# Performance work log

Measured on AMD Instinct MI355X. Metric: run time of the kernel, lower is better.

Reference implementation:

```python
import jax, jax.numpy as jnp
import numpy as np

CIN, HID, OUT = 128, 256, 349
NTYPES, ETYPES = 4, 5
N0, N1, N2 = 120000, 40000, 10000
GNODES, GEDGES = 250000, 2000000
E0, E1 = 1500000, 400000


def setup_inputs() -> dict:
    key = jax.random.key(0)
    ks = jax.random.split(key, 24)
    ri = jax.random.randint
    rn = jax.random.normal
    inp = {}
    inp['n_id'] = ri(ks[0], (N0,), 0, GNODES)
    inp['x0'] = rn(ks[1], (100000, CIN), dtype=jnp.float32)
    inp['src0'] = ri(ks[2], (E0,), 0, N0)
    inp['dst0'] = ri(ks[3], (E0,), 0, N1)
    inp['e_id0'] = ri(ks[4], (E0,), 0, GEDGES)
    inp['src1'] = ri(ks[5], (E1,), 0, N1)
    inp['dst1'] = ri(ks[6], (E1,), 0, N2)
    inp['e_id1'] = ri(ks[7], (E1,), 0, GEDGES)
    inp['edge_type'] = ri(ks[8], (GEDGES,), 0, ETYPES)
    inp['node_type'] = ri(ks[9], (GNODES,), 0, NTYPES)
    inp['local_node_idx'] = ri(ks[10], (GNODES,), 0, 50000)
    # learned parameters
    inp['emb1'] = rn(ks[11], (50000, CIN), dtype=jnp.float32)
    inp['emb2'] = rn(ks[12], (50000, CIN), dtype=jnp.float32)
    inp['emb3'] = rn(ks[13], (50000, CIN), dtype=jnp.float32)
    s0 = 1.0 / np.sqrt(CIN)
    s1 = 1.0 / np.sqrt(HID)
    inp['relW0'] = rn(ks[14], (ETYPES, CIN, HID), dtype=jnp.float32) * s0
    inp['rootW0'] = rn(ks[15], (NTYPES, CIN, HID), dtype=jnp.float32) * s0
    inp['rootb0'] = rn(ks[16], (NTYPES, HID), dtype=jnp.float32) * 0.02
    inp['relW1'] = rn(ks[17], (ETYPES, HID, OUT), dtype=jnp.float32) * s1
    inp['rootW1'] = rn(ks[18], (NTYPES, HID, OUT), dtype=jnp.float32) * s1
    inp['rootb1'] = rn(ks[19], (NTYPES, OUT), dtype=jnp.float32) * 0.02
    return inp


def _group_input(tables, node_type, local_node_idx, n_id):
    # RGNN.group_input: per-node-type gather from feature / embedding tables.
    nt = node_type[n_id]            # [N0]
    li = local_node_idx[n_id]       # [N0]
    h = jnp.zeros((n_id.shape[0], CIN), dtype=tables[0].dtype)
    for k, tab in enumerate(tables):
        idx = jnp.minimum(li, tab.shape[0] - 1)
        h = jnp.where((nt == k)[:, None], tab[idx], h)
    return h, nt


def _rgcn_layer(x, nt_src, src, dst, et, relW, rootW, rootb, n_tgt):
    # out = sum_t mean-aggregate(x_j over edges of type t) @ W_t  (linear commutes with mean)
    T = relW.shape[0]
    xj = x[src]                                           # [E, Cin] gather
    seg = dst * T + et                                    # fused (target, edge_type) segment id
    sums = jax.ops.segment_sum(xj, seg, num_segments=n_tgt * T)
    cnts = jax.ops.segment_sum(jnp.ones((src.shape[0],), x.dtype), seg, num_segments=n_tgt * T)
    mean = (sums / jnp.maximum(cnts, 1.0)[:, None]).reshape(n_tgt, T, -1)  # [Nt, T, Cin]
    out = jnp.einsum('ntc,tco->no', mean, relW)           # [Nt, Cout]
    # per-node-type root linear: out[mask] += root_lins[i](x_target[mask])
    x_t = x[:n_tgt]
    nt_t = nt_src[:n_tgt]
    allr = jnp.einsum('nc,tco->tno', x_t, rootW) + rootb[:, None, :]  # [Tn, Nt, Cout]
    root = jnp.take_along_axis(allr, nt_t[None, :, None], axis=0)[0]
    return out + root


def reference(n_id, x0, src0, dst0, e_id0, src1, dst1, e_id1, edge_type, node_type,
              local_node_idx, emb1, emb2, emb3, relW0, rootW0, rootb0, relW1, rootW1, rootb1):
    h, nt = _group_input([x0, emb1, emb2, emb3], node_type, local_node_idx, n_id)
    # layer 0: I -> H
    h = _rgcn_layer(h, nt, src0, dst0, edge_type[e_id0], relW0, rootW0, rootb0, N1)
    h = jax.nn.relu(h)
    nt = nt[:N1]
    # layer 1: H -> O
    h = _rgcn_layer(h, nt, src1, dst1, edge_type[e_id1], relW1, rootW1, rootb1, N2)
    return jax.nn.log_softmax(h, axis=-1)
```

## Files before the change

### kernel.cpp

```cpp
#include <hip/hip_runtime.h>
#include <hip/hip_bf16.h>
#include <cmath>

constexpr int kCIN = 128, kHID = 256, kOUT = 349;
constexpr int kNT = 4, kET = 5;
constexpr int kN0 = 120000, kN1 = 40000, kN2 = 10000;
constexpr int kNSEG0 = kN1 * kET;
constexpr int kNSEG1 = kN2 * kET;
constexpr int kNSEG = kNSEG0 + kNSEG1;

constexpr int kBinSegs = 512;
constexpr int kNBin0 = (kNSEG0 + kBinSegs - 1) / kBinSegs;
constexpr int kNBin1 = (kNSEG1 + kBinSegs - 1) / kBinSegs;
constexpr int kNBin  = kNBin0 + kNBin1;
constexpr int kNBLK  = 512;
constexpr int kSB    = 128;

typedef __bf16 bf16x8 __attribute__((ext_vector_type(8)));
typedef float f32x4 __attribute__((ext_vector_type(4)));
typedef float f32x2v __attribute__((ext_vector_type(2)));
typedef unsigned short ushort8v __attribute__((ext_vector_type(8)));

__device__ __forceinline__ unsigned short f2b(float f) {
    unsigned int b = __float_as_uint(f);
    unsigned int r = (b + 0x7FFFu + ((b >> 16) & 1u)) >> 16;
    return (unsigned short)r;
}
__device__ __forceinline__ float b2f(unsigned short u) {
    return __uint_as_float((unsigned int)u << 16);
}
__device__ __forceinline__ void gl2lds16(const void* g, void* l) {
    __builtin_amdgcn_global_load_lds(
        (const __attribute__((address_space(1))) void*)g,
        (__attribute__((address_space(3))) void*)l, 16, 0, 0);
}

__device__ __forceinline__ unsigned int f2e4m3(float f) {
#if __has_builtin(__builtin_amdgcn_cvt_pk_fp8_f32)
    return (unsigned int)(__builtin_amdgcn_cvt_pk_fp8_f32(f, f, 0, false) & 0xFF);
#else
    unsigned int sb = (__float_as_uint(f) >> 31) << 7;
    float m = fminf(fabsf(f), 448.f);
    unsigned int code;
    if (m < 0.015625f) {
        code = (unsigned int)__float2int_rn(m * 512.f);
    } else {
        unsigned int b = __float_as_uint(m);
        b = b + 0x7FFFF + ((b >> 20) & 1);
        int e8 = (int)(b >> 23) - 120;
        if (e8 > 15) code = 0x7E;
        else code = ((unsigned int)e8 << 3) | ((b >> 20) & 7);
    }
    return sb | code;
#endif
}

__device__ __forceinline__ void e4m3x4_to_f32(unsigned int u, float* o4) {
#if __has_builtin(__builtin_amdgcn_cvt_pk_f32_fp8)
    f32x2v a = __builtin_amdgcn_cvt_pk_f32_fp8(u, false);
    f32x2v b = __builtin_amdgcn_cvt_pk_f32_fp8(u, true);
    o4[0] = a[0]; o4[1] = a[1]; o4[2] = b[0]; o4[3] = b[1];
#else
#pragma unroll
    for (int i = 0; i < 4; i++) {
        unsigned int c = (u >> (8 * i)) & 0xFF;
        unsigned int s = c >> 7, e = (c >> 3) & 15, mm = c & 7;
        float v;
        if (e == 0) v = (float)mm * 0.001953125f;
        else        v = __uint_as_float((e + 120u) << 23 | mm << 20);
        o4[i] = s ? -v : v;
    }
#endif
}

__global__ void k_prep(const float* __restrict__ relW0, const float* __restrict__ rootW0,
                       unsigned short* __restrict__ Bt0T,
                       const float* __restrict__ relW1, const float* __restrict__ rootW1,
                       unsigned short* __restrict__ Bt1T,
                       const int* __restrict__ etype, unsigned char* __restrict__ et8, int nET)
{
    constexpr int T0 = kNT * 256 * 768;
    constexpr int T1 = kNT * 384 * 1536;
    constexpr int TP = T0 + T1;
    int i = blockIdx.x * 256 + threadIdx.x;
    if (i < T0) {
        int g = i / (256 * 768);
        int rem = i - g * (256 * 768);
        int col = rem / 768;
        int k = rem - col * 768;
        float v = (k < 640) ? relW0[(size_t)k * 256 + col]
                            : rootW0[((size_t)g * 128 + (k - 640)) * 256 + col];
        Bt0T[i] = f2b(v);
    } else if (i < TP) {
        int ii = i - T0;
        int g = ii / (384 * 1536);
        int rem = ii - g * (384 * 1536);
        int col = rem / 1536;
        int k = rem - col * 1536;
        float v = 0.f;
        if (col < kOUT) v = (k < 1280) ? relW1[(size_t)k * kOUT + col]
                                       : rootW1[((size_t)g * 256 + (k - 1280)) * kOUT + col];
        Bt1T[ii] = f2b(v);
    } else {
        int k = i - TP;
        if (k < nET) et8[k] = (unsigned char)etype[k];
    }
}

__global__ void k_gather(const int* __restrict__ n_id, const float* __restrict__ x0,
                         const float* __restrict__ e1, const float* __restrict__ e2,
                         const float* __restrict__ e3, const int* __restrict__ ntype,
                         const int* __restrict__ lidx, unsigned short* __restrict__ h0b,
                         unsigned char* __restrict__ h0f8, int* __restrict__ nt0)
{
    int row = blockIdx.x * 8 + (threadIdx.x >> 5);
    if (row >= kN0) return;
    int lane = threadIdx.x & 31;
    int gid = n_id[row];
    int nt = ntype[gid];
    int li = lidx[gid];
    const float* tab;
    int rows;
    if (nt == 0)      { tab = x0; rows = 100000; }
    else if (nt == 1) { tab = e1; rows = 50000; }
    else if (nt == 2) { tab = e2; rows = 50000; }
    else              { tab = e3; rows = 50000; }
    int idx = li < rows ? li : rows - 1;
    float4 v = reinterpret_cast<const float4*>(tab + (size_t)idx * kCIN)[lane];
    ushort4 o;
    o.x = f2b(v.x); o.y = f2b(v.y); o.z = f2b(v.z); o.w = f2b(v.w);
    reinterpret_cast<ushort4*>(h0b + (size_t)row * kCIN)[lane] = o;
    unsigned int q = f2e4m3(v.x) | (f2e4m3(v.y) << 8) | (f2e4m3(v.z) << 16) | (f2e4m3(v.w) << 24);
    reinterpret_cast<unsigned int*>(h0f8 + (size_t)row * kCIN)[lane] = q;
    if (lane == 0) nt0[row] = nt;
}

__global__ __launch_bounds__(1024) void k_bincnt(
    const int* __restrict__ dst0, const int* __restrict__ eid0, int E0,
    const int* __restrict__ dst1, const int* __restrict__ eid1, int E1,
    const unsigned char* __restrict__ et8, int* __restrict__ cnts2d,
    int* __restrict__ seg32,
    const int* __restrict__ nt0, int* __restrict__ ntcnts)
{
    __shared__ int h[kNBin];
    const int tid = threadIdx.x;
    if (blockIdx.x < kNBLK) {
        for (int k = tid; k < kNBin; k += 1024) h[k] = 0;
        __syncthreads();
        int Etot = E0 + E1;
        int chunk = (Etot + kNBLK - 1) / kNBLK;
        int lo = blockIdx.x * chunk;
        int hi = min(lo + chunk, Etot);
        for (int i = lo + tid; i < hi; i += 1024) {
            int c;
            if (i < E0) c = dst0[i] * kET + (int)et8[eid0[i]];
            else { int e = i - E0; c = kNBin0 * kBinSegs + dst1[e] * kET + (int)et8[eid1[e]]; }
            seg32[i] = c;
            atomicAdd(&h[c >> 9], 1);
        }
        __syncthreads();
        for (int k = tid; k < kNBin; k += 1024) cnts2d[(size_t)k * kNBLK + blockIdx.x] = h[k];
    } else {
        int b = blockIdx.x - kNBLK;
        int layer = b >= kSB;
        int blk = b - layer * kSB;
        int M = layer ? kN2 : kN1;
        if (tid < 4) h[tid] = 0;
        __syncthreads();
        int chunk = (M + kSB - 1) / kSB;
        int lo = blk * chunk, hi = min(lo + chunk, M);
        for (int i = lo + tid; i < hi; i += 1024) atomicAdd(&h[nt0[i]], 1);
        __syncthreads();
        if (tid < 4) ntcnts[(layer * 4 + tid) * kSB + blk] = h[tid];
    }
}

__global__ void k_scan1(const int* __restrict__ cnt, int* __restrict__ excl,
                        int* __restrict__ blksum, int n)
{
    __shared__ int sm[1024];
    int i = blockIdx.x * 1024 + threadIdx.x;
    int v = (i < n) ? cnt[i] : 0;
    sm[threadIdx.x] = v;
    __syncthreads();
    for (int off = 1; off < 1024; off <<= 1) {
        int t = (threadIdx.x >= off) ? sm[threadIdx.x - off] : 0;
        __syncthreads();
        sm[threadIdx.x] += t;
        __syncthreads();
    }
    if (i < n) excl[i] = sm[threadIdx.x] - v;
    if (threadIdx.x == 1023) blksum[blockIdx.x] = sm[1023];
}

__global__ __launch_bounds__(1024) void k_scan2(
    int* __restrict__ blksum, int nblk,
    const int* __restrict__ ntcnts, int* __restrict__ ntoffs,
    int* __restrict__ goff0, int* __restrict__ goff1)
{
    __shared__ int sm[1024];
    int tid = threadIdx.x;
    if (blockIdx.x == 0) {
        int v = (tid < nblk) ? blksum[tid] : 0;
        sm[tid] = v;
        __syncthreads();
        for (int off = 1; off < 1024; off <<= 1) {
            int t = (tid >= off) ? sm[tid - off] : 0;
            __syncthreads();
            sm[tid] += t;
            __syncthreads();
        }
        if (tid < nblk) blksum[tid] = sm[tid] - v;
    } else {
        int v = ntcnts[tid];
        sm[tid] = v;
        __syncthreads();
        for (int off = 1; off < 512; off <<= 1) {
            int t = 0;
            if ((tid & 511) >= off) t = sm[tid - off];
            __syncthreads();
            sm[tid] += t;
            __syncthreads();
        }
        int excl = sm[tid] - v;
        ntoffs[tid] = excl;
        if ((tid & 127) == 0) {
            int layer = tid >> 9;
            int t = (tid >> 7) & 3;
            if (layer == 0) goff0[t] = excl; else goff1[t] = excl;
        }
        if (tid == 0) { goff0[4] = kN1; goff1[4] = kN2; }
    }
}

__global__ __launch_bounds__(1024) void k_binplace(
    const int* __restrict__ src0, int E0,
    const int* __restrict__ src1, int E1,
    const int* __restrict__ seg32,
    const int* __restrict__ offs2d, const int* __restrict__ blksum,
    unsigned int* __restrict__ pairs,
    const int* __restrict__ nt0, const int* __restrict__ ntoffs,
    int* __restrict__ perm0, int* __restrict__ perm1)
{
    __shared__ int cur[kNBin];
    const int tid = threadIdx.x;
    if (blockIdx.x < kNBLK) {
        for (int k = tid; k < kNBin; k += 1024) {
            size_t li = (size_t)k * kNBLK + blockIdx.x;
            cur[k] = offs2d[li] + blksum[li >> 10];
        }
        __syncthreads();
        int Etot = E0 + E1;
        int chunk = (Etot + kNBLK - 1) / kNBLK;
        int lo = blockIdx.x * chunk;
        int hi = min(lo + chunk, Etot);
        for (int i = lo + tid; i < hi; i += 1024) {
            int c = seg32[i];
            int s = (i < E0) ? src0[i] : src1[i - E0];
            unsigned int pay = (unsigned int)s | ((unsigned int)(c & (kBinSegs - 1)) << 17);
            int p = atomicAdd(&cur[c >> 9], 1);
            pairs[p] = pay;
        }
    } else {
        int b = blockIdx.x - kNBLK;
        int layer = b >= kSB;
        int blk = b - layer * kSB;
        int M = layer ? kN2 : kN1;
        int* perm = layer ? perm1 : perm0;
        if (tid < 4) cur[tid] = ntoffs[(layer * 4 + tid) * kSB + blk];
        __syncthreads();
        int chunk = (M + kSB - 1) / kSB;
        int lo = blk * chunk, hi = min(lo + chunk, M);
        for (int i = lo + tid; i < hi; i += 1024) {
            int p = atomicAdd(&cur[nt0[i]], 1);
            perm[p] = i;
        }
    }
}

__global__ __launch_bounds__(1024) void k_binscatter(
    const int* __restrict__ offs2d, const int* __restrict__ blksum, int Etot,
    const unsigned int* __restrict__ pairs,
    int* __restrict__ order, int* __restrict__ starts, int* __restrict__ cnt)
{
    __shared__ int h[kBinSegs];
    __shared__ int sc[kBinSegs];
    __shared__ int cur[kBinSegs];
    const int bin = blockIdx.x;
    const int tid = threadIdx.x;
    size_t bi = (size_t)bin * kNBLK;
    const int base = offs2d[bi] + blksum[bi >> 10];
    int end = Etot;
    if (bin + 1 < kNBin) {
        size_t ei = (size_t)(bin + 1) * kNBLK;
        end = offs2d[ei] + blksum[ei >> 10];
    }
    const int c = end - base;
    const unsigned int* pp = pairs + base;

    for (int k = tid; k < kBinSegs; k += 1024) h[k] = 0;
    __syncthreads();
    for (int j = tid; j < c; j += 1024) atomicAdd(&h[pp[j] >> 17], 1);
    __syncthreads();
    if (tid < kBinSegs) sc[tid] = h[tid];
    __syncthreads();
    for (int off = 1; off < kBinSegs; off <<= 1) {
        int t = 0;
        if (tid < kBinSegs && tid >= off) t = sc[tid - off];
        __syncthreads();
        if (tid < kBinSegs) sc[tid] += t;
        __syncthreads();
    }
    int seg_rel, abs_base, seglim;
    if (bin < kNBin0) { seg_rel = bin * kBinSegs; abs_base = seg_rel; seglim = kNSEG0 - seg_rel; }
    else { seg_rel = (bin - kNBin0) * kBinSegs; abs_base = kNSEG0 + seg_rel; seglim = kNSEG1 - seg_rel; }
    if (tid < kBinSegs) {
        int excl = sc[tid] - h[tid];
        cur[tid] = excl;
        if (tid < seglim) {
            starts[abs_base + tid] = base + excl;
            cnt[abs_base + tid] = h[tid];
        }
    }
    __syncthreads();
    for (int j = tid; j < c; j += 1024) {
        unsigned int u = pp[j];
        int sl = (int)(u >> 17);
        int p = atomicAdd(&cur[sl], 1);
        order[base + p] = (int)(u & 0x1FFFFu);
    }
}

template<int C>
__global__ __launch_bounds__(256) void k_segreduce8(
    const int* __restrict__ starts, const int* __restrict__ cnt,
    const int* __restrict__ order, const unsigned char* __restrict__ h8,
    unsigned short* __restrict__ mean, int nseg)
{
    constexpr int L = C / 16;
    constexpr int SPB = 256 / L;
    int sidx = blockIdx.x * SPB + threadIdx.x / L;
    if (sidx >= nseg) return;
    int lane = threadIdx.x % L;
    int st = starts[sidx];
    int n = cnt[sidx];
    const unsigned char* hp = h8 + (size_t)lane * 16;
    float a0[16], a1[16];
#pragma unroll
    for (int i = 0; i < 16; i++) { a0[i] = 0.f; a1[i] = 0.f; }
    int j = 0;
    for (; j + 2 <= n; j += 2) {
        int s0 = order[st + j + 0];
        int s1 = order[st + j + 1];
        uint4 u0 = *reinterpret_cast<const uint4*>(hp + (size_t)s0 * C);
        uint4 u1 = *reinterpret_cast<const uint4*>(hp + (size_t)s1 * C);
        float d[16];
        e4m3x4_to_f32(u0.x, d); e4m3x4_to_f32(u0.y, d + 4);
        e4m3x4_to_f32(u0.z, d + 8); e4m3x4_to_f32(u0.w, d + 12);
#pragma unroll
        for (int i = 0; i < 16; i++) a0[i] += d[i];
        e4m3x4_to_f32(u1.x, d); e4m3x4_to_f32(u1.y, d + 4);
        e4m3x4_to_f32(u1.z, d + 8); e4m3x4_to_f32(u1.w, d + 12);
#pragma unroll
        for (int i = 0; i < 16; i++) a1[i] += d[i];
    }
    if (j < n) {
        int s0 = order[st + j];
        uint4 u0 = *reinterpret_cast<const uint4*>(hp + (size_t)s0 * C);
        float d[16];
        e4m3x4_to_f32(u0.x, d); e4m3x4_to_f32(u0.y, d + 4);
        e4m3x4_to_f32(u0.z, d + 8); e4m3x4_to_f32(u0.w, d + 12);
#pragma unroll
        for (int i = 0; i < 16; i++) a0[i] += d[i];
    }
    float sc = 1.0f / fmaxf((float)n, 1.0f);
    ushort8v o0, o1;
#pragma unroll
    for (int i = 0; i < 8; i++) {
        o0[i] = f2b((a0[i] + a1[i]) * sc);
        o1[i] = f2b((a0[i + 8] + a1[i + 8]) * sc);
    }
    unsigned short* mp = mean + (size_t)sidx * C + lane * 16;
    *reinterpret_cast<ushort8v*>(mp) = o0;
    *reinterpret_cast<ushort8v*>(mp + 8) = o1;
}

template<int C, int BM, int BN, int RELU, int OUTBF16, int OUTF8>
__global__ __launch_bounds__(256) void k_gemm_sorted(
    int M, int Nreal, int NpadK,
    const unsigned short* __restrict__ meanb,
    const unsigned short* __restrict__ hb,
    const unsigned short* __restrict__ BtT,
    const float* __restrict__ rootb,
    const int* __restrict__ perm, const int* __restrict__ goff,
    unsigned short* __restrict__ outb, float* __restrict__ outf,
    unsigned char* __restrict__ outf8)
{
    constexpr int K1 = kET * C;
    constexpr int K  = K1 + C;
    constexpr int FM = BM / 32;
    constexpr int FN = BN / 32;
    __shared__ __align__(16) char ldsA[BM * 128];
    __shared__ __align__(16) char ldsB[BN * 128];

    int g, row0s = 0, gend = 0;
    {
        int gs0 = goff[0], gs1 = goff[1], gs2 = goff[2], gs3 = goff[3], gs4 = goff[4];
        int gs[5] = {gs0, gs1, gs2, gs3, gs4};
        int t = blockIdx.x, tb = 0;
        for (g = 0; g < 4; ++g) {
            int cg = gs[g + 1] - gs[g];
            int ntl = (cg + BM - 1) / BM;
            if (t < tb + ntl) { row0s = gs[g] + (t - tb) * BM; gend = gs[g + 1]; break; }
            tb += ntl;
        }
        if (g == 4) return;
    }
    const int rows_here = min(BM, gend - row0s);
    const unsigned short* BtG = BtT + (size_t)g * NpadK;

    const int tid = threadIdx.x;
    const int col0 = blockIdx.y * BN;
    const int wid = tid >> 6, lane = tid & 63;
    const int wrow = (wid >> 1) * (BM / 2);
    const int wcol = (wid & 1) * (BN / 2);
    const int lr = lane >> 3;
    const int kb = (lane & 7) * 16;

    f32x4 acc[FM][FN] = {};

    for (int k0 = 0; k0 < K; k0 += 64) {
        const bool inMean = (k0 < K1);
        const size_t kB = (size_t)k0 * 2;
#pragma unroll
        for (int c2 = 0; c2 < BM / 32; ++c2) {
            int rb = (wid * (BM / 32) + c2) * 8;
            int r = rb + lr;
            int pr = perm[row0s + min(r, rows_here - 1)];
            const char* rowp = inMean
                ? (const char*)(meanb + (size_t)pr * K1) + kB
                : (const char*)(hb + (size_t)pr * C) + (kB - (size_t)K1 * 2);
            gl2lds16(rowp + (kb ^ ((r & 7) << 4)), &ldsA[rb * 128]);
        }
#pragma unroll
        for (int c2 = 0; c2 < BN / 32; ++c2) {
            int rb = (wid * (BN / 32) + c2) * 8;
            int r = rb + lr;
            const char* rowp = (const char*)(BtG + (size_t)(col0 + r) * K) + kB;
            gl2lds16(rowp + (kb ^ ((r & 7) << 4)), &ldsB[rb * 128]);
        }
        __syncthreads();
#pragma unroll
        for (int kc = 0; kc < 2; kc++) {
            int kb2 = kc * 64 + (lane >> 4) * 16;
            bf16x8 af[FM], bfr[FN];
#pragma unroll
            for (int m = 0; m < FM; m++) {
                int r = wrow + m * 16 + (lane & 15);
                af[m] = *reinterpret_cast<const bf16x8*>(&ldsA[r * 128 + (kb2 ^ ((r & 7) << 4))]);
            }
#pragma unroll
            for (int n = 0; n < FN; n++) {
                int r = wcol + n * 16 + (lane & 15);
                bfr[n] = *reinterpret_cast<const bf16x8*>(&ldsB[r * 128 + (kb2 ^ ((r & 7) << 4))]);
            }
#pragma unroll
            for (int m = 0; m < FM; m++)
#pragma unroll
                for (int n = 0; n < FN; n++)
                    acc[m][n] = __builtin_amdgcn_mfma_f32_16x16x32_bf16(af[m], bfr[n], acc[m][n], 0, 0, 0);
        }
        __syncthreads();
    }

#pragma unroll
    for (int m = 0; m < FM; m++) {
        int rlb = wrow + m * 16 + (lane >> 4) * 4;
#pragma unroll
        for (int n = 0; n < FN; n++) {
            int col = col0 + wcol + n * 16 + (lane & 15);
            if (col >= Nreal) continue;
            f32x4 v = acc[m][n];
#pragma unroll
            for (int j = 0; j < 4; j++) {
                int rl = rlb + j;
                if (rl >= rows_here) continue;
                int orig = perm[row0s + rl];
                float x = v[j] + rootb[g * Nreal + col];
                if (RELU) x = fmaxf(x, 0.f);
                if (OUTBF16) {
                    outb[(size_t)orig * Nreal + col] = f2b(x);
                    if (OUTF8) outf8[(size_t)orig * Nreal + col] = (unsigned char)f2e4m3(x);
                } else {
                    outf[(size_t)orig * Nreal + col] = x;
                }
            }
        }
    }
}

__global__ void k_logsm(float* __restrict__ out, int M, int N)
{
    int row = blockIdx.x * 4 + (threadIdx.x >> 6);
    if (row >= M) return;
    int lane = threadIdx.x & 63;
    float* p = out + (size_t)row * N;
    float mx = -3.4e38f;
    for (int c = lane; c < N; c += 64) mx = fmaxf(mx, p[c]);
#pragma unroll
    for (int o = 32; o > 0; o >>= 1) mx = fmaxf(mx, __shfl_xor(mx, o));
    float s = 0.f;
    for (int c = lane; c < N; c += 64) s += expf(p[c] - mx);
#pragma unroll
    for (int o = 32; o > 0; o >>= 1) s += __shfl_xor(s, o);
    float lse = mx + logf(s);
    for (int c = lane; c < N; c += 64) p[c] -= lse;
}

extern "C" void kernel_launch(void* const* d_in, const int* in_sizes, int n_in,
                              void* d_out, int out_size, void* d_ws, size_t ws_size,
                              hipStream_t stream)
{
    const int*   n_id   = (const int*)d_in[0];
    const float* x0     = (const float*)d_in[1];
    const int*   src0   = (const int*)d_in[2];
    const int*   dst0   = (const int*)d_in[3];
    const int*   eid0   = (const int*)d_in[4];
    const int*   src1   = (const int*)d_in[5];
    const int*   dst1   = (const int*)d_in[6];
    const int*   eid1   = (const int*)d_in[7];
    const int*   etype  = (const int*)d_in[8];
    const int*   ntype  = (const int*)d_in[9];
    const int*   lidx   = (const int*)d_in[10];
    const float* emb1   = (const float*)d_in[11];
    const float* emb2   = (const float*)d_in[12];
    const float* emb3   = (const float*)d_in[13];
    const float* relW0  = (const float*)d_in[14];
    const float* rootW0 = (const float*)d_in[15];
    const float* rootb0 = (const float*)d_in[16];
    const float* relW1  = (const float*)d_in[17];
    const float* rootW1 = (const float*)d_in[18];
    const float* rootb1 = (const float*)d_in[19];
    float* out = (float*)d_out;

    const int E0 = in_sizes[2];
    const int E1 = in_sizes[5];
    const int Etot = E0 + E1;
    const int nET = in_sizes[8];
    constexpr int K0s  = kET * kCIN + kCIN;
    constexpr int K1s  = kET * kHID + kHID;
    constexpr int Npad0 = 256;
    constexpr int Npad1 = 384;

    char* ws = (char*)d_ws;
    size_t off = 0;
    auto alloc = [&](size_t bytes) -> void* {
        void* p = ws + off;
        off = (off + bytes + 255) & ~(size_t)255;
        return p;
    };
    unsigned short* h0b   = (unsigned short*)alloc((size_t)kN0 * kCIN * 2);
    unsigned char*  h0f8  = (unsigned char*)alloc((size_t)kN0 * kCIN);
    int*            nt0   = (int*)alloc((size_t)kN0 * 4);
    unsigned short* meanb = (unsigned short*)alloc((size_t)kNSEG0 * kCIN * 2);
    int*            cnt    = (int*)alloc((size_t)kNSEG * 4);
    int*            starts = (int*)alloc((size_t)kNSEG * 4);
    int*            cnts2d = (int*)alloc((size_t)kNBin * kNBLK * 4);
    int*            offs2d = (int*)alloc((size_t)kNBin * kNBLK * 4);
    int*            blksum = (int*)alloc(1024 * 4);
    unsigned int*   pairs  = (unsigned int*)alloc((size_t)Etot * 4);
    int*            order  = (int*)alloc((size_t)Etot * 4);
    int*            seg32  = (int*)alloc((size_t)Etot * 4);
    unsigned char*  et8    = (unsigned char*)alloc((size_t)nET);
    unsigned short* h1b   = (unsigned short*)alloc((size_t)kN1 * kHID * 2);
    unsigned char*  h1f8  = (unsigned char*)alloc((size_t)kN1 * kHID);
    unsigned short* Bt0T  = (unsigned short*)alloc((size_t)kNT * Npad0 * K0s * 2);
    unsigned short* Bt1T  = (unsigned short*)alloc((size_t)kNT * Npad1 * K1s * 2);
    int*            perm0  = (int*)alloc((size_t)kN1 * 4);
    int*            goff0  = (int*)alloc(8 * 4);
    int*            perm1  = (int*)alloc((size_t)kN2 * 4);
    int*            goff1  = (int*)alloc(8 * 4);
    int*            ntcnts = (int*)alloc(1024 * 4);
    int*            ntoffs = (int*)alloc(1024 * 4);

    constexpr int TPREP = kNT * Npad0 * K0s + kNT * Npad1 * K1s;
    int prep_total = TPREP + nET;
    k_prep<<<(prep_total + 255) / 256, 256, 0, stream>>>(relW0, rootW0, Bt0T, relW1, rootW1, Bt1T,
                                                         etype, et8, nET);
    k_gather<<<(kN0 + 7) / 8, 256, 0, stream>>>(n_id, x0, emb1, emb2, emb3, ntype, lidx, h0b, h0f8, nt0);

    k_bincnt<<<kNBLK + 2 * kSB, 1024, 0, stream>>>(dst0, eid0, E0, dst1, eid1, E1, et8,
                                                   cnts2d, seg32, nt0, ntcnts);
    int nscan = kNBin * kNBLK;
    int nblk = (nscan + 1023) / 1024;
    k_scan1<<<nblk, 1024, 0, stream>>>(cnts2d, offs2d, blksum, nscan);
    k_scan2<<<2, 1024, 0, stream>>>(blksum, nblk, ntcnts, ntoffs, goff0, goff1);
    k_binplace<<<kNBLK + 2 * kSB, 1024, 0, stream>>>(src0, E0, src1, E1, seg32,
                                                     offs2d, blksum, pairs, nt0, ntoffs, perm0, perm1);
    k_binscatter<<<kNBin, 1024, 0, stream>>>(offs2d, blksum, Etot, pairs, order, starts, cnt);

    k_segreduce8<kCIN><<<(kNSEG0 + 31) / 32, 256, 0, stream>>>(starts, cnt, order, h0f8, meanb, kNSEG0);
    dim3 g0(kN1 / 64 + 4, Npad0 / 128);
    k_gemm_sorted<kCIN, 64, 128, 1, 1, 1><<<g0, 256, 0, stream>>>(
        kN1, kHID, Npad0 * K0s, meanb, h0b, Bt0T, rootb0, perm0, goff0, h1b, nullptr, h1f8);

    k_segreduce8<kHID><<<(kNSEG1 + 15) / 16, 256, 0, stream>>>(starts + kNSEG0, cnt + kNSEG0, order, h1f8, meanb, kNSEG1);
    dim3 g1(kN2 / 64 + 5, Npad1 / 128);
    k_gemm_sorted<kHID, 64, 128, 0, 0, 0><<<g1, 256, 0, stream>>>(
        kN2, kOUT, Npad1 * K1s, meanb, h1b, Bt1T, rootb1, perm1, goff1, nullptr, out, nullptr);

    k_logsm<<<(kN2 + 3) / 4, 256, 0, stream>>>(out, kN2, kOUT);
}
```

Baseline: 244.5 us.

## Widen layer-0 GEMM tile to full N and remap blocks for XCD-aware locality

```diff
diff --git a/kernel.cpp b/kernel.cpp
--- a/kernel.cpp
+++ b/kernel.cpp
@@ -385,7 +385,7 @@
     *reinterpret_cast<ushort8v*>(mp + 8) = o1;
 }
 
-template<int C, int BM, int BN, int RELU, int OUTBF16, int OUTF8>
+template<int C, int BM, int BNF, int NCB, int WR, int WC, int RELU, int OUTBF16, int OUTF8>
 __global__ __launch_bounds__(256) void k_gemm_sorted(
     int M, int Nreal, int NpadK,
     const unsigned short* __restrict__ meanb,
@@ -398,16 +398,22 @@
 {
     constexpr int K1 = kET * C;
     constexpr int K  = K1 + C;
-    constexpr int FM = BM / 32;
-    constexpr int FN = BN / 32;
+    constexpr int FM = BM / (16 * WR);
+    constexpr int FN = BNF / (16 * WC);
     __shared__ __align__(16) char ldsA[BM * 128];
-    __shared__ __align__(16) char ldsB[BN * 128];
+    __shared__ __align__(16) char ldsB[BNF * 128];
+
+    int nwg = gridDim.x;
+    int orig = blockIdx.x;
+    int q = nwg >> 3, r8 = nwg & 7, x8 = orig & 7;
+    int logical = (x8 < r8 ? x8 * (q + 1) : r8 * (q + 1) + (x8 - r8) * q) + (orig >> 3);
+    int colb = logical % NCB;
+    int t = logical / NCB;
 
     int g, row0s = 0, gend = 0;
     {
-        int gs0 = goff[0], gs1 = goff[1], gs2 = goff[2], gs3 = goff[3], gs4 = goff[4];
-        int gs[5] = {gs0, gs1, gs2, gs3, gs4};
-        int t = blockIdx.x, tb = 0;
+        int gs[5] = {goff[0], goff[1], goff[2], goff[3], goff[4]};
+        int tb = 0;
         for (g = 0; g < 4; ++g) {
             int cg = gs[g + 1] - gs[g];
             int ntl = (cg + BM - 1) / BM;
@@ -420,10 +426,10 @@
     const unsigned short* BtG = BtT + (size_t)g * NpadK;
 
     const int tid = threadIdx.x;
-    const int col0 = blockIdx.y * BN;
+    const int col0 = colb * BNF;
     const int wid = tid >> 6, lane = tid & 63;
-    const int wrow = (wid >> 1) * (BM / 2);
-    const int wcol = (wid & 1) * (BN / 2);
+    const int wrow = (wid / WC) * (BM / WR);
+    const int wcol = (wid % WC) * (BNF / WC);
     const int lr = lane >> 3;
     const int kb = (lane & 7) * 16;
 
@@ -443,8 +449,8 @@
             gl2lds16(rowp + (kb ^ ((r & 7) << 4)), &ldsA[rb * 128]);
         }
 #pragma unroll
-        for (int c2 = 0; c2 < BN / 32; ++c2) {
-            int rb = (wid * (BN / 32) + c2) * 8;
+        for (int c2 = 0; c2 < BNF / 32; ++c2) {
+            int rb = (wid * (BNF / 32) + c2) * 8;
             int r = rb + lr;
             const char* rowp = (const char*)(BtG + (size_t)(col0 + r) * K) + kB;
             gl2lds16(rowp + (kb ^ ((r & 7) << 4)), &ldsB[rb * 128]);
@@ -485,14 +491,14 @@
             for (int j = 0; j < 4; j++) {
                 int rl = rlb + j;
                 if (rl >= rows_here) continue;
-                int orig = perm[row0s + rl];
-                float x = v[j] + rootb[g * Nreal + col];
-                if (RELU) x = fmaxf(x, 0.f);
+                int orig_row = perm[row0s + rl];
+                float xv = v[j] + rootb[g * Nreal + col];
+                if (RELU) xv = fmaxf(xv, 0.f);
                 if (OUTBF16) {
-                    outb[(size_t)orig * Nreal + col] = f2b(x);
-                    if (OUTF8) outf8[(size_t)orig * Nreal + col] = (unsigned char)f2e4m3(x);
+                    outb[(size_t)orig_row * Nreal + col] = f2b(xv);
+                    if (OUTF8) outf8[(size_t)orig_row * Nreal + col] = (unsigned char)f2e4m3(xv);
                 } else {
-                    outf[(size_t)orig * Nreal + col] = x;
+                    outf[(size_t)orig_row * Nreal + col] = xv;
                 }
             }
         }
@@ -600,13 +606,13 @@
     k_binscatter<<<kNBin, 1024, 0, stream>>>(offs2d, blksum, Etot, pairs, order, starts, cnt);
 
     k_segreduce8<kCIN><<<(kNSEG0 + 31) / 32, 256, 0, stream>>>(starts, cnt, order, h0f8, meanb, kNSEG0);
-    dim3 g0(kN1 / 64 + 4, Npad0 / 128);
-    k_gemm_sorted<kCIN, 64, 128, 1, 1, 1><<<g0, 256, 0, stream>>>(
+    int g0 = kN1 / 64 + 4;
+    k_gemm_sorted<kCIN, 64, 256, 1, 2, 2, 1, 1, 1><<<g0, 256, 0, stream>>>(
         kN1, kHID, Npad0 * K0s, meanb, h0b, Bt0T, rootb0, perm0, goff0, h1b, nullptr, h1f8);
 
     k_segreduce8<kHID><<<(kNSEG1 + 15) / 16, 256, 0, stream>>>(starts + kNSEG0, cnt + kNSEG0, order, h1f8, meanb, kNSEG1);
-    dim3 g1(kN2 / 64 + 5, Npad1 / 128);
-    k_gemm_sorted<kHID, 64, 128, 0, 0, 0><<<g1, 256, 0, stream>>>(
+    int g1 = (kN2 / 64 + 5) * 3;
+    k_gemm_sorted<kHID, 64, 128, 3, 2, 2, 0, 0, 0><<<g1, 256, 0, stream>>>(
         kN2, kOUT, Npad1 * K1s, meanb, h1b, Bt1T, rootb1, perm1, goff1, nullptr, out, nullptr);
 
     k_logsm<<<(kN2 + 3) / 4, 256, 0, stream>>>(out, kN2, kOUT);
```

New measurement: 260.9 us. 1.07x slower.
